# Kernel tuning notes

Hardware: AMD Instinct MI355X
Metric: run time of the kernel (lower is better)

## Reference

```python
import jax, jax.numpy as jnp
import numpy as np

E, T, D_IN, D_H = 8, 2048, 2048, 5632


def setup_inputs() -> dict:
    key = jax.random.key(0)
    kx, kg, kd, ku = jax.random.split(key, 4)
    scale = 0.02  # init_std-like scaling for weights
    return {
        "x": jax.random.normal(kx, (E, T, D_IN), dtype=jnp.float32),
        "gate_proj": jax.random.normal(kg, (E, D_IN, D_H), dtype=jnp.float32) * scale,
        "down_proj": jax.random.normal(kd, (E, D_IN, D_H), dtype=jnp.float32) * scale,
        "up_proj": jax.random.normal(ku, (E, D_H, D_IN), dtype=jnp.float32) * scale,
        "tokens_per_expert": T,
    }


def reference(x, gate_proj, down_proj, up_proj, tokens_per_expert):
    # ep_size=1: dispatch/combine are identity. Grouped SwiGLU per expert.
    # x: [E, T, d_in]; gate/down: [E, d_in, d_h]; up: [E, d_h, d_in]
    g = jnp.einsum('etd,edh->eth', x, gate_proj)
    u = jnp.einsum('etd,edh->eth', x, down_proj)
    h = jax.nn.silu(g) * u  # [E, T, d_h]
    out = jnp.einsum('eth,ehd->etd', h, up_proj)  # [E, T, d_in]
    return out
```

## Files before the change

### kernel.cpp

```cpp
#include <hip/hip_runtime.h>
#include <hip/hip_bf16.h>


#define NEXP 8
#define TT   2048
#define DIN  2048
#define DH   5632

using short8 = __attribute__((ext_vector_type(8))) short;
using f32x4  = __attribute__((ext_vector_type(4))) float;

static __device__ __forceinline__ float bf2f(unsigned short u) {
    return __uint_as_float(((unsigned int)u) << 16);
}
static __device__ __forceinline__ unsigned short f2bf(float f) {
    unsigned int i = __float_as_uint(f);
    return (unsigned short)((i + 0x7FFFu + ((i >> 16) & 1u)) >> 16);
}
static __device__ __forceinline__ void gld16(const void* g, void* l) {
    __builtin_amdgcn_global_load_lds(
        (const __attribute__((address_space(1))) void*)g,
        (__attribute__((address_space(3))) void*)l, 16, 0, 0);
}

__global__ __launch_bounds__(512, 2) void gemm_gu(
    const unsigned short* __restrict__ Xb,
    const unsigned short* __restrict__ Wgt,
    const unsigned short* __restrict__ Wdt,
    unsigned short* __restrict__ Hb)
{
    __shared__ __align__(16) unsigned short lds[65536];

    const int tid  = threadIdx.x;
    const int wave = tid >> 6, lane = tid & 63;
    const int l15 = lane & 15, l4 = lane >> 4;
    const int wr = wave >> 2, wc = wave & 3;

    const int bid = blockIdx.x;
    const int e   = bid & 7;
    const int cu  = bid >> 3;
    const int m0  = (cu & 7) * 256;
    const int nb  = cu >> 3;

    const int K = DIN;

    const unsigned short* Ae = Xb  + (size_t)e * TT * DIN;
    const unsigned short* Gbase = Wgt + (size_t)e * DH * DIN;
    const unsigned short* Dbase = Wdt + (size_t)e * DH * DIN;
    unsigned short* He = Hb + (size_t)e * TT * DH;

    const int c0 = tid, c1 = 512 + tid;
    const int cs0 = c0 ^ ((c0 >> 3) & 7), cs1 = c1 ^ ((c1 >> 3) & 7);
    const int row0 = cs0 >> 3, col0 = (cs0 & 7) * 8;
    const int row1 = cs1 >> 3, col1 = (cs1 & 7) * 8;

    int ibA[4][2], ibB[2][2];
#pragma unroll
    for (int s = 0; s < 4; ++s)
#pragma unroll
        for (int ks = 0; ks < 2; ++ks) {
            const int r = wr * 64 + s * 16 + l15;
            ibA[s][ks] = (r * 128 + ks * 64 + l4 * 16) ^ ((r & 7) << 4);
        }
#pragma unroll
    for (int s = 0; s < 2; ++s)
#pragma unroll
        for (int ks = 0; ks < 2; ++ks) {
            const int r = wc * 32 + s * 16 + l15;
            ibB[s][ks] = (r * 128 + ks * 64 + l4 * 16) ^ ((r & 7) << 4);
        }

    f32x4 acc[8][4] = {};
    short8 Aq[4][2], Gq[2][2], Dq[2][2];

    auto stageA = [&](int ro, int kk, int slot) {
        gld16(Ae + (size_t)(m0 + ro + row0) * K + (kk + col0), &lds[slot * 8192 + wave * 512]);
        gld16(Ae + (size_t)(m0 + ro + row1) * K + (kk + col1), &lds[slot * 8192 + 4096 + wave * 512]);
    };
    auto stageW = [&](const unsigned short* p, int kk, int slot) {
        gld16(p + (size_t)row0 * K + (kk + col0), &lds[slot * 8192 + wave * 512]);
        gld16(p + (size_t)row1 * K + (kk + col1), &lds[slot * 8192 + 4096 + wave * 512]);
    };

    const size_t NSTEP = (size_t)512 * K;
    const unsigned short* Gc = Gbase + (size_t)(nb * 128) * K;
    const unsigned short* Dc = Dbase + (size_t)(nb * 128) * K;

    stageA(0, 0, 0);  stageW(Gc, 0, 1);  stageW(Dc, 0, 2);  stageA(128, 0, 3);
    stageA(0, 64, 4); stageW(Gc, 64, 5); stageW(Dc, 64, 6);
    asm volatile("s_waitcnt vmcnt(6)" ::: "memory");
    asm volatile("s_barrier" ::: "memory");

    const char* ldsc = (const char*)lds;
    for (int i = 0; i < 11; ++i) {
        const unsigned short* Gn = Gc + NSTEP;
        const unsigned short* Dn = Dc + NSTEP;
        for (int t = 0; t < 32; ++t) {
            const int g = (i << 5) + t;
            const int sA0 = ((4 * g + 0) & 7) * 16384;
            const int sG  = ((4 * g + 1) & 7) * 16384;
            const int sD  = ((4 * g + 2) & 7) * 16384;
            const int sA1 = ((4 * g + 3) & 7) * 16384;

#pragma unroll
            for (int s = 0; s < 4; ++s) {
                Aq[s][0] = *(const short8*)(ldsc + sA0 + ibA[s][0]);
                Aq[s][1] = *(const short8*)(ldsc + sA0 + ibA[s][1]);
            }
#pragma unroll
            for (int s = 0; s < 2; ++s) {
                Gq[s][0] = *(const short8*)(ldsc + sG + ibB[s][0]);
                Gq[s][1] = *(const short8*)(ldsc + sG + ibB[s][1]);
            }
            if (i < 10 || t + 1 < 32)
                stageA(128, ((t + 1) & 31) * 64, (4 * g + 7) & 7);
            asm volatile("s_barrier" ::: "memory");
            asm volatile("s_waitcnt lgkmcnt(0)" ::: "memory");
            __builtin_amdgcn_sched_barrier(0);
            __builtin_amdgcn_s_setprio(1);
#pragma unroll
            for (int m = 0; m < 4; ++m)
#pragma unroll
                for (int n = 0; n < 2; ++n) {
                    acc[m][n] = __builtin_amdgcn_mfma_f32_16x16x32_bf16(Aq[m][0], Gq[n][0], acc[m][n], 0, 0, 0);
                    acc[m][n] = __builtin_amdgcn_mfma_f32_16x16x32_bf16(Aq[m][1], Gq[n][1], acc[m][n], 0, 0, 0);
                }
            __builtin_amdgcn_s_setprio(0);
            asm volatile("s_barrier" ::: "memory");

#pragma unroll
            for (int s = 0; s < 2; ++s) {
                Dq[s][0] = *(const short8*)(ldsc + sD + ibB[s][0]);
                Dq[s][1] = *(const short8*)(ldsc + sD + ibB[s][1]);
            }
            if (i < 10 || t + 2 < 32)
                stageA(0, ((t + 2) & 31) * 64, (4 * g + 8) & 7);
            asm volatile("s_barrier" ::: "memory");
            asm volatile("s_waitcnt lgkmcnt(0)" ::: "memory");
            __builtin_amdgcn_sched_barrier(0);
            __builtin_amdgcn_s_setprio(1);
#pragma unroll
            for (int m = 0; m < 4; ++m)
#pragma unroll
                for (int n = 0; n < 2; ++n) {
                    acc[m][2 + n] = __builtin_amdgcn_mfma_f32_16x16x32_bf16(Aq[m][0], Dq[n][0], acc[m][2 + n], 0, 0, 0);
                    acc[m][2 + n] = __builtin_amdgcn_mfma_f32_16x16x32_bf16(Aq[m][1], Dq[n][1], acc[m][2 + n], 0, 0, 0);
                }
            __builtin_amdgcn_s_setprio(0);
            asm volatile("s_barrier" ::: "memory");

#pragma unroll
            for (int s = 0; s < 4; ++s) {
                Aq[s][0] = *(const short8*)(ldsc + sA1 + ibA[s][0]);
                Aq[s][1] = *(const short8*)(ldsc + sA1 + ibA[s][1]);
            }
            if (i < 10 || t + 2 < 32)
                stageW((t + 2 < 32) ? Gc : Gn, ((t + 2) & 31) * 64, (4 * g + 9) & 7);
            asm volatile("s_barrier" ::: "memory");
            asm volatile("s_waitcnt lgkmcnt(0)" ::: "memory");
            __builtin_amdgcn_sched_barrier(0);
            __builtin_amdgcn_s_setprio(1);
#pragma unroll
            for (int m = 0; m < 4; ++m)
#pragma unroll
                for (int n = 0; n < 2; ++n) {
                    acc[4 + m][2 + n] = __builtin_amdgcn_mfma_f32_16x16x32_bf16(Aq[m][0], Dq[n][0], acc[4 + m][2 + n], 0, 0, 0);
                    acc[4 + m][2 + n] = __builtin_amdgcn_mfma_f32_16x16x32_bf16(Aq[m][1], Dq[n][1], acc[4 + m][2 + n], 0, 0, 0);
                }
            __builtin_amdgcn_s_setprio(0);
            asm volatile("s_barrier" ::: "memory");

            if (i < 10 || t + 2 < 32)
                stageW((t + 2 < 32) ? Dc : Dn, ((t + 2) & 31) * 64, (4 * g + 10) & 7);
            asm volatile("s_barrier" ::: "memory");
            __builtin_amdgcn_s_setprio(1);
#pragma unroll
            for (int m = 0; m < 4; ++m)
#pragma unroll
                for (int n = 0; n < 2; ++n) {
                    acc[4 + m][n] = __builtin_amdgcn_mfma_f32_16x16x32_bf16(Aq[m][0], Gq[n][0], acc[4 + m][n], 0, 0, 0);
                    acc[4 + m][n] = __builtin_amdgcn_mfma_f32_16x16x32_bf16(Aq[m][1], Gq[n][1], acc[4 + m][n], 0, 0, 0);
                }
            __builtin_amdgcn_s_setprio(0);
            if (g < 350)       asm volatile("s_waitcnt vmcnt(6)" ::: "memory");
            else if (g == 350) asm volatile("s_waitcnt vmcnt(0)" ::: "memory");
            asm volatile("s_barrier" ::: "memory");
        }

        const int n0i = (4 * i + nb) * 128;
#pragma unroll
        for (int fm = 0; fm < 8; ++fm) {
            const int row_b = m0 + (fm >> 2) * 128 + wr * 64 + (fm & 3) * 16 + l4 * 4;
#pragma unroll
            for (int nr = 0; nr < 2; ++nr) {
                const int col = n0i + wc * 32 + nr * 16 + l15;
#pragma unroll
                for (int j = 0; j < 4; ++j) {
                    const float gv = acc[fm][nr][j];
                    const float uv = acc[fm][2 + nr][j];
                    const float h = gv / (1.f + __expf(-gv)) * uv;
                    He[(size_t)(row_b + j) * DH + col] = f2bf(h);
                }
            }
        }
#pragma unroll
        for (int m = 0; m < 8; ++m)
#pragma unroll
            for (int n = 0; n < 4; ++n)
                acc[m][n] = (f32x4){0.f, 0.f, 0.f, 0.f};
        Gc = Gn; Dc = Dn;
    }
}

__global__ __launch_bounds__(512, 2) void gemm_out(
    const unsigned short* __restrict__ Ab,
    const unsigned short* __restrict__ Btb,
    float* __restrict__ Cf)
{
    __shared__ __align__(16) unsigned short lds[65536];

    const int tid  = threadIdx.x;
    const int wave = tid >> 6, lane = tid & 63;
    const int l15 = lane & 15, l4 = lane >> 4;
    const int wr = wave >> 2, wc = wave & 3;

    const int bid = blockIdx.x;
    const int e   = bid & 7;
    const int cu  = bid >> 3;
    const int m0  = (cu & 7) * 256;
    const int nb  = cu >> 3;

    const int N = DIN, K = DH, NT = K >> 6;
    const unsigned short* Ae = Ab  + (size_t)e * TT * DH;
    const unsigned short* Bbase = Btb + (size_t)e * DIN * DH;

    const int c0 = tid, c1 = 512 + tid;
    const int cs0 = c0 ^ ((c0 >> 3) & 7), cs1 = c1 ^ ((c1 >> 3) & 7);
    const int row0 = cs0 >> 3, col0 = (cs0 & 7) * 8;
    const int row1 = cs1 >> 3, col1 = (cs1 & 7) * 8;

    int ibA[4][2], ibB[2][2];
#pragma unroll
    for (int s = 0; s < 4; ++s)
#pragma unroll
        for (int ks = 0; ks < 2; ++ks) {
            const int r = wr * 64 + s * 16 + l15;
            ibA[s][ks] = (r * 128 + ks * 64 + l4 * 16) ^ ((r & 7) << 4);
        }
#pragma unroll
    for (int s = 0; s < 2; ++s)
#pragma unroll
        for (int ks = 0; ks < 2; ++ks) {
            const int r = wc * 32 + s * 16 + l15;
            ibB[s][ks] = (r * 128 + ks * 64 + l4 * 16) ^ ((r & 7) << 4);
        }

    f32x4 acc[8][4] = {};
    short8 Aq[4][2], B0q[2][2], B1q[2][2];

    auto stageA = [&](int ro, int kk, int slot) {
        gld16(Ae + (size_t)(m0 + ro + row0) * K + (kk + col0), &lds[slot * 8192 + wave * 512]);
        gld16(Ae + (size_t)(m0 + ro + row1) * K + (kk + col1), &lds[slot * 8192 + 4096 + wave * 512]);
    };
    auto stageB = [&](const unsigned short* base, int co, int kk, int slot) {
        gld16(base + (size_t)(co + row0) * K + (kk + col0), &lds[slot * 8192 + wave * 512]);
        gld16(base + (size_t)(co + row1) * K + (kk + col1), &lds[slot * 8192 + 4096 + wave * 512]);
    };

    const size_t NSTEP = (size_t)1024 * K;
    const unsigned short* Bc = Bbase + (size_t)(nb * 256) * K;

    stageA(0, 0, 0); stageB(Bc, 0, 0, 1); stageB(Bc, 128, 0, 2); stageA(128, 0, 3);
    stageA(0, 64, 4); stageB(Bc, 0, 64, 5); stageB(Bc, 128, 64, 6);
    asm volatile("s_waitcnt vmcnt(6)" ::: "memory");
    asm volatile("s_barrier" ::: "memory");

    const char* ldsc = (const char*)lds;
    for (int i = 0; i < 2; ++i) {
        const unsigned short* Bn = Bc + NSTEP;
        for (int t = 0; t < 88; ++t) {
            const int g = i * 88 + t;
            const int sA0 = ((4 * g + 0) & 7) * 16384;
            const int sB0 = ((4 * g + 1) & 7) * 16384;
            const int sB1 = ((4 * g + 2) & 7) * 16384;
            const int sA1 = ((4 * g + 3) & 7) * 16384;

#pragma unroll
            for (int s = 0; s < 4; ++s) {
                Aq[s][0] = *(const short8*)(ldsc + sA0 + ibA[s][0]);
                Aq[s][1] = *(const short8*)(ldsc + sA0 + ibA[s][1]);
            }
#pragma unroll
            for (int s = 0; s < 2; ++s) {
                B0q[s][0] = *(const short8*)(ldsc + sB0 + ibB[s][0]);
                B0q[s][1] = *(const short8*)(ldsc + sB0 + ibB[s][1]);
            }
            {
                const int tt = t + 1;
                if (i < 1 || tt < 88)
                    stageA(128, (tt >= 88 ? tt - 88 : tt) * 64, (4 * g + 7) & 7);
            }
            asm volatile("s_barrier" ::: "memory");
            asm volatile("s_waitcnt lgkmcnt(0)" ::: "memory");
            __builtin_amdgcn_sched_barrier(0);
            __builtin_amdgcn_s_setprio(1);
#pragma unroll
            for (int m = 0; m < 4; ++m)
#pragma unroll
                for (int n = 0; n < 2; ++n) {
                    acc[m][n] = __builtin_amdgcn_mfma_f32_16x16x32_bf16(Aq[m][0], B0q[n][0], acc[m][n], 0, 0, 0);
                    acc[m][n] = __builtin_amdgcn_mfma_f32_16x16x32_bf16(Aq[m][1], B0q[n][1], acc[m][n], 0, 0, 0);
                }
            __builtin_amdgcn_s_setprio(0);
            asm volatile("s_barrier" ::: "memory");

#pragma unroll
            for (int s = 0; s < 2; ++s) {
                B1q[s][0] = *(const short8*)(ldsc + sB1 + ibB[s][0]);
                B1q[s][1] = *(const short8*)(ldsc + sB1 + ibB[s][1]);
            }
            {
                const int tt = t + 2;
                if (i < 1 || tt < 88)
                    stageA(0, (tt >= 88 ? tt - 88 : tt) * 64, (4 * g + 8) & 7);
            }
            asm volatile("s_barrier" ::: "memory");
            asm volatile("s_waitcnt lgkmcnt(0)" ::: "memory");
            __builtin_amdgcn_sched_barrier(0);
            __builtin_amdgcn_s_setprio(1);
#pragma unroll
            for (int m = 0; m < 4; ++m)
#pragma unroll
                for (int n = 0; n < 2; ++n) {
                    acc[m][2 + n] = __builtin_amdgcn_mfma_f32_16x16x32_bf16(Aq[m][0], B1q[n][0], acc[m][2 + n], 0, 0, 0);
                    acc[m][2 + n] = __builtin_amdgcn_mfma_f32_16x16x32_bf16(Aq[m][1], B1q[n][1], acc[m][2 + n], 0, 0, 0);
                }
            __builtin_amdgcn_s_setprio(0);
            asm volatile("s_barrier" ::: "memory");

#pragma unroll
            for (int s = 0; s < 4; ++s) {
                Aq[s][0] = *(const short8*)(ldsc + sA1 + ibA[s][0]);
                Aq[s][1] = *(const short8*)(ldsc + sA1 + ibA[s][1]);
            }
            {
                const int tt = t + 2;
                if (i < 1 || tt < 88)
                    stageB((tt >= 88 ? Bn : Bc), 0, (tt >= 88 ? tt - 88 : tt) * 64, (4 * g + 9) & 7);
            }
            asm volatile("s_barrier" ::: "memory");
            asm volatile("s_waitcnt lgkmcnt(0)" ::: "memory");
            __builtin_amdgcn_sched_barrier(0);
            __builtin_amdgcn_s_setprio(1);
#pragma unroll
            for (int m = 0; m < 4; ++m)
#pragma unroll
                for (int n = 0; n < 2; ++n) {
                    acc[4 + m][2 + n] = __builtin_amdgcn_mfma_f32_16x16x32_bf16(Aq[m][0], B1q[n][0], acc[4 + m][2 + n], 0, 0, 0);
                    acc[4 + m][2 + n] = __builtin_amdgcn_mfma_f32_16x16x32_bf16(Aq[m][1], B1q[n][1], acc[4 + m][2 + n], 0, 0, 0);
                }
            __builtin_amdgcn_s_setprio(0);
            asm volatile("s_barrier" ::: "memory");

            {
                const int tt = t + 2;
                if (i < 1 || tt < 88)
                    stageB((tt >= 88 ? Bn : Bc), 128, (tt >= 88 ? tt - 88 : tt) * 64, (4 * g + 10) & 7);
            }
            asm volatile("s_barrier" ::: "memory");
            __builtin_amdgcn_s_setprio(1);
#pragma unroll
            for (int m = 0; m < 4; ++m)
#pragma unroll
                for (int n = 0; n < 2; ++n) {
                    acc[4 + m][n] = __builtin_amdgcn_mfma_f32_16x16x32_bf16(Aq[m][0], B0q[n][0], acc[4 + m][n], 0, 0, 0);
                    acc[4 + m][n] = __builtin_amdgcn_mfma_f32_16x16x32_bf16(Aq[m][1], B0q[n][1], acc[4 + m][n], 0, 0, 0);
                }
            __builtin_amdgcn_s_setprio(0);
            if (g < 174)       asm volatile("s_waitcnt vmcnt(6)" ::: "memory");
            else if (g == 174) asm volatile("s_waitcnt vmcnt(0)" ::: "memory");
            asm volatile("s_barrier" ::: "memory");
        }

        const int n0i = (4 * i + nb) * 256;
        float* Ce = Cf + (size_t)e * TT * DIN;
#pragma unroll
        for (int fm = 0; fm < 8; ++fm) {
            const int row_b = (fm >> 2) * 128 + wr * 64 + (fm & 3) * 16 + l4 * 4;
#pragma unroll
            for (int fn = 0; fn < 4; ++fn) {
                const int col = n0i + (fn >> 1) * 128 + wc * 32 + (fn & 1) * 16 + l15;
#pragma unroll
                for (int j = 0; j < 4; ++j)
                    Ce[(size_t)(m0 + row_b + j) * N + col] = acc[fm][fn][j];
            }
        }
#pragma unroll
        for (int m = 0; m < 8; ++m)
#pragma unroll
            for (int n = 0; n < 4; ++n)
                acc[m][n] = (f32x4){0.f, 0.f, 0.f, 0.f};
        Bc = Bn;
    }
}

__global__ __launch_bounds__(256) void transpose_f32_bf16(
    const float* __restrict__ in, unsigned short* __restrict__ out,
    int R, int C, size_t ies, size_t oes)
{
    in  += (size_t)blockIdx.z * ies;
    out += (size_t)blockIdx.z * oes;
    __shared__ unsigned short t[64][65];
    const int tid = threadIdx.x;
    const int lr = tid >> 4, lc = (tid & 15) * 4;
    const int r0 = blockIdx.y * 64, c0 = blockIdx.x * 64;
#pragma unroll
    for (int i = 0; i < 4; ++i) {
        const int row = lr + i * 16;
        const float4 v = *(const float4*)(in + (size_t)(r0 + row) * C + c0 + lc);
        t[row][lc + 0] = f2bf(v.x); t[row][lc + 1] = f2bf(v.y);
        t[row][lc + 2] = f2bf(v.z); t[row][lc + 3] = f2bf(v.w);
    }
    __syncthreads();
#pragma unroll
    for (int i = 0; i < 4; ++i) {
        const int crow = lr + i * 16;
        ushort4 wv;
        wv.x = t[lc + 0][crow]; wv.y = t[lc + 1][crow];
        wv.z = t[lc + 2][crow]; wv.w = t[lc + 3][crow];
        *(ushort4*)(out + (size_t)(c0 + crow) * R + r0 + lc) = wv;
    }
}

__global__ __launch_bounds__(256) void conv_f32_bf16(
    const float* __restrict__ in, unsigned short* __restrict__ out, int n4)
{
    int i = blockIdx.x * 256 + threadIdx.x;
    const int stride = gridDim.x * 256;
    for (; i < n4; i += stride) {
        const float4 v = ((const float4*)in)[i];
        ushort4 wv;
        wv.x = f2bf(v.x); wv.y = f2bf(v.y); wv.z = f2bf(v.z); wv.w = f2bf(v.w);
        ((ushort4*)out)[i] = wv;
    }
}

extern "C" void kernel_launch(void* const* d_in, const int* in_sizes, int n_in,
                              void* d_out, int out_size, void* d_ws, size_t ws_size,
                              hipStream_t stream)
{
    const float* x  = (const float*)d_in[0];
    const float* wg = (const float*)d_in[1];
    const float* wd = (const float*)d_in[2];
    const float* wu = (const float*)d_in[3];
    float* out = (float*)d_out;

    const size_t XSZ = (size_t)TT * DIN;
    const size_t WSZ = (size_t)DIN * DH;
    unsigned short* xb  = (unsigned short*)d_ws;
    unsigned short* wgt = xb  + (size_t)NEXP * XSZ;
    unsigned short* wdt = wgt + (size_t)NEXP * WSZ;
    unsigned short* hb  = wdt + (size_t)NEXP * WSZ;

    conv_f32_bf16<<<4096, 256, 0, stream>>>(x, xb, (int)(NEXP * XSZ / 4));
    transpose_f32_bf16<<<dim3(DH / 64, DIN / 64, NEXP), 256, 0, stream>>>(
        wg, wgt, DIN, DH, WSZ, WSZ);
    transpose_f32_bf16<<<dim3(DH / 64, DIN / 64, NEXP), 256, 0, stream>>>(
        wd, wdt, DIN, DH, WSZ, WSZ);
    gemm_gu<<<256, 512, 0, stream>>>(xb, wgt, wdt, hb);
    transpose_f32_bf16<<<dim3(DIN / 64, DH / 64, NEXP), 256, 0, stream>>>(
        wu, wgt, DH, DIN, WSZ, WSZ);
    gemm_out<<<256, 512, 0, stream>>>(hb, wgt, out);
}
```

Baseline: 1.297 ms.

## Grow LDS ring to ten slots and cut per-step barriers from eight to two

Both GEMM kernels move from an 8-slot to a 10-slot LDS ring buffer, indexed by a running modulo-10 counter. The extra slots let the next global-to-LDS stages be issued without waiting for readers. Both B fragments are now loaded together at the start of each step, and the MFMA phases are merged, so only two workgroup barriers remain per step instead of eight. This raises LDS per block from 128 KB to 160 KB, which may stop two 512-thread blocks fitting per CU. It also depends on the widened ring for correctness against write-after-read hazards.

```diff
diff --git a/kernel.cpp b/kernel.cpp
--- a/kernel.cpp
+++ b/kernel.cpp
@@ -10,9 +10,6 @@
 using short8 = __attribute__((ext_vector_type(8))) short;
 using f32x4  = __attribute__((ext_vector_type(4))) float;
 
-static __device__ __forceinline__ float bf2f(unsigned short u) {
-    return __uint_as_float(((unsigned int)u) << 16);
-}
 static __device__ __forceinline__ unsigned short f2bf(float f) {
     unsigned int i = __float_as_uint(f);
     return (unsigned short)((i + 0x7FFFu + ((i >> 16) & 1u)) >> 16);
@@ -29,7 +26,7 @@
     const unsigned short* __restrict__ Wdt,
     unsigned short* __restrict__ Hb)
 {
-    __shared__ __align__(16) unsigned short lds[65536];
+    __shared__ __align__(16) unsigned short lds[81920];
 
     const int tid  = threadIdx.x;
     const int wave = tid >> 6, lane = tid & 63;
@@ -45,8 +42,6 @@
     const int K = DIN;
 
     const unsigned short* Ae = Xb  + (size_t)e * TT * DIN;
-    const unsigned short* Gbase = Wgt + (size_t)e * DH * DIN;
-    const unsigned short* Dbase = Wdt + (size_t)e * DH * DIN;
     unsigned short* He = Hb + (size_t)e * TT * DH;
 
     const int c0 = tid, c1 = 512 + tid;
@@ -73,34 +68,41 @@
     f32x4 acc[8][4] = {};
     short8 Aq[4][2], Gq[2][2], Dq[2][2];
 
-    auto stageA = [&](int ro, int kk, int slot) {
-        gld16(Ae + (size_t)(m0 + ro + row0) * K + (kk + col0), &lds[slot * 8192 + wave * 512]);
-        gld16(Ae + (size_t)(m0 + ro + row1) * K + (kk + col1), &lds[slot * 8192 + 4096 + wave * 512]);
+    char* ldsb = (char*)lds;
+    auto stageA = [&](int ro, int kk, int so) {
+        gld16(Ae + (size_t)(m0 + ro + row0) * K + (kk + col0), ldsb + so + wave * 1024);
+        gld16(Ae + (size_t)(m0 + ro + row1) * K + (kk + col1), ldsb + so + 8192 + wave * 1024);
     };
-    auto stageW = [&](const unsigned short* p, int kk, int slot) {
-        gld16(p + (size_t)row0 * K + (kk + col0), &lds[slot * 8192 + wave * 512]);
-        gld16(p + (size_t)row1 * K + (kk + col1), &lds[slot * 8192 + 4096 + wave * 512]);
+    auto stageW = [&](const unsigned short* p, int kk, int so) {
+        gld16(p + (size_t)row0 * K + (kk + col0), ldsb + so + wave * 1024);
+        gld16(p + (size_t)row1 * K + (kk + col1), ldsb + so + 8192 + wave * 1024);
     };
+    auto w10 = [](int x) { return x >= 10 ? x - 10 : x; };
 
     const size_t NSTEP = (size_t)512 * K;
-    const unsigned short* Gc = Gbase + (size_t)(nb * 128) * K;
-    const unsigned short* Dc = Dbase + (size_t)(nb * 128) * K;
-
-    stageA(0, 0, 0);  stageW(Gc, 0, 1);  stageW(Dc, 0, 2);  stageA(128, 0, 3);
-    stageA(0, 64, 4); stageW(Gc, 64, 5); stageW(Dc, 64, 6);
+    const unsigned short* Gc = Wgt + (size_t)e * DH * DIN + (size_t)(nb * 128) * K;
+    const unsigned short* Dc = Wdt + (size_t)e * DH * DIN + (size_t)(nb * 128) * K;
+
+    stageA(0, 0, 0 << 14);  stageW(Gc, 0, 1 << 14);  stageW(Dc, 0, 2 << 14);  stageA(128, 0, 3 << 14);
+    stageA(0, 64, 4 << 14); stageW(Gc, 64, 5 << 14); stageW(Dc, 64, 6 << 14);
     asm volatile("s_waitcnt vmcnt(6)" ::: "memory");
     asm volatile("s_barrier" ::: "memory");
 
     const char* ldsc = (const char*)lds;
+    int q = 0;
     for (int i = 0; i < 11; ++i) {
         const unsigned short* Gn = Gc + NSTEP;
         const unsigned short* Dn = Dc + NSTEP;
         for (int t = 0; t < 32; ++t) {
             const int g = (i << 5) + t;
-            const int sA0 = ((4 * g + 0) & 7) * 16384;
-            const int sG  = ((4 * g + 1) & 7) * 16384;
-            const int sD  = ((4 * g + 2) & 7) * 16384;
-            const int sA1 = ((4 * g + 3) & 7) * 16384;
+            const int sA0 = q << 14;
+            const int sG  = w10(q + 1) << 14;
+            const int sD  = w10(q + 2) << 14;
+            const int sA1 = w10(q + 3) << 14;
+            const int stA1 = w10(q + 7) << 14;
+            const int stA0 = w10(q + 8) << 14;
+            const int stG  = w10(q + 9) << 14;
+            const int stD  = sA0;
 
 #pragma unroll
             for (int s = 0; s < 4; ++s) {
@@ -111,10 +113,11 @@
             for (int s = 0; s < 2; ++s) {
                 Gq[s][0] = *(const short8*)(ldsc + sG + ibB[s][0]);
                 Gq[s][1] = *(const short8*)(ldsc + sG + ibB[s][1]);
+                Dq[s][0] = *(const short8*)(ldsc + sD + ibB[s][0]);
+                Dq[s][1] = *(const short8*)(ldsc + sD + ibB[s][1]);
             }
             if (i < 10 || t + 1 < 32)
-                stageA(128, ((t + 1) & 31) * 64, (4 * g + 7) & 7);
-            asm volatile("s_barrier" ::: "memory");
+                stageA(128, ((t + 1) & 31) * 64, stA1);
             asm volatile("s_waitcnt lgkmcnt(0)" ::: "memory");
             __builtin_amdgcn_sched_barrier(0);
             __builtin_amdgcn_s_setprio(1);
@@ -126,18 +129,8 @@
                     acc[m][n] = __builtin_amdgcn_mfma_f32_16x16x32_bf16(Aq[m][1], Gq[n][1], acc[m][n], 0, 0, 0);
                 }
             __builtin_amdgcn_s_setprio(0);
-            asm volatile("s_barrier" ::: "memory");
-
-#pragma unroll
-            for (int s = 0; s < 2; ++s) {
-                Dq[s][0] = *(const short8*)(ldsc + sD + ibB[s][0]);
-                Dq[s][1] = *(const short8*)(ldsc + sD + ibB[s][1]);
-            }
             if (i < 10 || t + 2 < 32)
-                stageA(0, ((t + 2) & 31) * 64, (4 * g + 8) & 7);
-            asm volatile("s_barrier" ::: "memory");
-            asm volatile("s_waitcnt lgkmcnt(0)" ::: "memory");
-            __builtin_amdgcn_sched_barrier(0);
+                stageA(0, ((t + 2) & 31) * 64, stA0);
             __builtin_amdgcn_s_setprio(1);
 #pragma unroll
             for (int m = 0; m < 4; ++m)
@@ -147,16 +140,13 @@
                     acc[m][2 + n] = __builtin_amdgcn_mfma_f32_16x16x32_bf16(Aq[m][1], Dq[n][1], acc[m][2 + n], 0, 0, 0);
                 }
             __builtin_amdgcn_s_setprio(0);
-            asm volatile("s_barrier" ::: "memory");
-
 #pragma unroll
             for (int s = 0; s < 4; ++s) {
                 Aq[s][0] = *(const short8*)(ldsc + sA1 + ibA[s][0]);
                 Aq[s][1] = *(const short8*)(ldsc + sA1 + ibA[s][1]);
             }
             if (i < 10 || t + 2 < 32)
-                stageW((t + 2 < 32) ? Gc : Gn, ((t + 2) & 31) * 64, (4 * g + 9) & 7);
-            asm volatile("s_barrier" ::: "memory");
+                stageW((t + 2 < 32) ? Gc : Gn, ((t + 2) & 31) * 64, stG);
             asm volatile("s_waitcnt lgkmcnt(0)" ::: "memory");
             __builtin_amdgcn_sched_barrier(0);
             __builtin_amdgcn_s_setprio(1);
@@ -167,13 +157,6 @@
                     acc[4 + m][2 + n] = __builtin_amdgcn_mfma_f32_16x16x32_bf16(Aq[m][0], Dq[n][0], acc[4 + m][2 + n], 0, 0, 0);
                     acc[4 + m][2 + n] = __builtin_amdgcn_mfma_f32_16x16x32_bf16(Aq[m][1], Dq[n][1], acc[4 + m][2 + n], 0, 0, 0);
                 }
-            __builtin_amdgcn_s_setprio(0);
-            asm volatile("s_barrier" ::: "memory");
-
-            if (i < 10 || t + 2 < 32)
-                stageW((t + 2 < 32) ? Dc : Dn, ((t + 2) & 31) * 64, (4 * g + 10) & 7);
-            asm volatile("s_barrier" ::: "memory");
-            __builtin_amdgcn_s_setprio(1);
 #pragma unroll
             for (int m = 0; m < 4; ++m)
 #pragma unroll
@@ -182,9 +165,13 @@
                     acc[4 + m][n] = __builtin_amdgcn_mfma_f32_16x16x32_bf16(Aq[m][1], Gq[n][1], acc[4 + m][n], 0, 0, 0);
                 }
             __builtin_amdgcn_s_setprio(0);
+            asm volatile("s_barrier" ::: "memory");
+            if (i < 10 || t + 2 < 32)
+                stageW((t + 2 < 32) ? Dc : Dn, ((t + 2) & 31) * 64, stD);
             if (g < 350)       asm volatile("s_waitcnt vmcnt(6)" ::: "memory");
             else if (g == 350) asm volatile("s_waitcnt vmcnt(0)" ::: "memory");
             asm volatile("s_barrier" ::: "memory");
+            q = w10(q + 4);
         }
 
         const int n0i = (4 * i + nb) * 128;
@@ -217,7 +204,7 @@
     const unsigned short* __restrict__ Btb,
     float* __restrict__ Cf)
 {
-    __shared__ __align__(16) unsigned short lds[65536];
+    __shared__ __align__(16) unsigned short lds[81920];
 
     const int tid  = threadIdx.x;
     const int wave = tid >> 6, lane = tid & 63;
@@ -230,9 +217,8 @@
     const int m0  = (cu & 7) * 256;
     const int nb  = cu >> 3;
 
-    const int N = DIN, K = DH, NT = K >> 6;
+    const int N = DIN, K = DH;
     const unsigned short* Ae = Ab  + (size_t)e * TT * DH;
-    const unsigned short* Bbase = Btb + (size_t)e * DIN * DH;
 
     const int c0 = tid, c1 = 512 + tid;
     const int cs0 = c0 ^ ((c0 >> 3) & 7), cs1 = c1 ^ ((c1 >> 3) & 7);
@@ -258,32 +244,39 @@
     f32x4 acc[8][4] = {};
     short8 Aq[4][2], B0q[2][2], B1q[2][2];
 
-    auto stageA = [&](int ro, int kk, int slot) {
-        gld16(Ae + (size_t)(m0 + ro + row0) * K + (kk + col0), &lds[slot * 8192 + wave * 512]);
-        gld16(Ae + (size_t)(m0 + ro + row1) * K + (kk + col1), &lds[slot * 8192 + 4096 + wave * 512]);
+    char* ldsb = (char*)lds;
+    auto stageA = [&](int ro, int kk, int so) {
+        gld16(Ae + (size_t)(m0 + ro + row0) * K + (kk + col0), ldsb + so + wave * 1024);
+        gld16(Ae + (size_t)(m0 + ro + row1) * K + (kk + col1), ldsb + so + 8192 + wave * 1024);
     };
-    auto stageB = [&](const unsigned short* base, int co, int kk, int slot) {
-        gld16(base + (size_t)(co + row0) * K + (kk + col0), &lds[slot * 8192 + wave * 512]);
-        gld16(base + (size_t)(co + row1) * K + (kk + col1), &lds[slot * 8192 + 4096 + wave * 512]);
+    auto stageB = [&](const unsigned short* base, int co, int kk, int so) {
+        gld16(base + (size_t)(co + row0) * K + (kk + col0), ldsb + so + wave * 1024);
+        gld16(base + (size_t)(co + row1) * K + (kk + col1), ldsb + so + 8192 + wave * 1024);
     };
+    auto w10 = [](int x) { return x >= 10 ? x - 10 : x; };
 
     const size_t NSTEP = (size_t)1024 * K;
-    const unsigned short* Bc = Bbase + (size_t)(nb * 256) * K;
-
-    stageA(0, 0, 0); stageB(Bc, 0, 0, 1); stageB(Bc, 128, 0, 2); stageA(128, 0, 3);
-    stageA(0, 64, 4); stageB(Bc, 0, 64, 5); stageB(Bc, 128, 64, 6);
+    const unsigned short* Bc = Btb + (size_t)e * DIN * DH + (size_t)(nb * 256) * K;
+
+    stageA(0, 0, 0 << 14); stageB(Bc, 0, 0, 1 << 14); stageB(Bc, 128, 0, 2 << 14); stageA(128, 0, 3 << 14);
+    stageA(0, 64, 4 << 14); stageB(Bc, 0, 64, 5 << 14); stageB(Bc, 128, 64, 6 << 14);
     asm volatile("s_waitcnt vmcnt(6)" ::: "memory");
     asm volatile("s_barrier" ::: "memory");
 
     const char* ldsc = (const char*)lds;
+    int q = 0;
     for (int i = 0; i < 2; ++i) {
         const unsigned short* Bn = Bc + NSTEP;
         for (int t = 0; t < 88; ++t) {
             const int g = i * 88 + t;
-            const int sA0 = ((4 * g + 0) & 7) * 16384;
-            const int sB0 = ((4 * g + 1) & 7) * 16384;
-            const int sB1 = ((4 * g + 2) & 7) * 16384;
-            const int sA1 = ((4 * g + 3) & 7) * 16384;
+            const int sA0 = q << 14;
+            const int sB0 = w10(q + 1) << 14;
+            const int sB1 = w10(q + 2) << 14;
+            const int sA1 = w10(q + 3) << 14;
+            const int stA1 = w10(q + 7) << 14;
+            const int stA0 = w10(q + 8) << 14;
+            const int stB0 = w10(q + 9) << 14;
+            const int stB1 = sA0;
 
 #pragma unroll
             for (int s = 0; s < 4; ++s) {
@@ -294,13 +287,14 @@
             for (int s = 0; s < 2; ++s) {
                 B0q[s][0] = *(const short8*)(ldsc + sB0 + ibB[s][0]);
                 B0q[s][1] = *(const short8*)(ldsc + sB0 + ibB[s][1]);
+                B1q[s][0] = *(const short8*)(ldsc + sB1 + ibB[s][0]);
+                B1q[s][1] = *(const short8*)(ldsc + sB1 + ibB[s][1]);
             }
             {
                 const int tt = t + 1;
                 if (i < 1 || tt < 88)
-                    stageA(128, (tt >= 88 ? tt - 88 : tt) * 64, (4 * g + 7) & 7);
-            }
-            asm volatile("s_barrier" ::: "memory");
+                    stageA(128, (tt >= 88 ? tt - 88 : tt) * 64, stA1);
+            }
             asm volatile("s_waitcnt lgkmcnt(0)" ::: "memory");
             __builtin_amdgcn_sched_barrier(0);
             __builtin_amdgcn_s_setprio(1);
@@ -312,21 +306,11 @@
                     acc[m][n] = __builtin_amdgcn_mfma_f32_16x16x32_bf16(Aq[m][1], B0q[n][1], acc[m][n], 0, 0, 0);
                 }
             __builtin_amdgcn_s_setprio(0);
-            asm volatile("s_barrier" ::: "memory");
-
-#pragma unroll
-            for (int s = 0; s < 2; ++s) {
-                B1q[s][0] = *(const short8*)(ldsc + sB1 + ibB[s][0]);
-                B1q[s][1] = *(const short8*)(ldsc + sB1 + ibB[s][1]);
-            }
             {
                 const int tt = t + 2;
                 if (i < 1 || tt < 88)
-                    stageA(0, (tt >= 88 ? tt - 88 : tt) * 64, (4 * g + 8) & 7);
-            }
-            asm volatile("s_barrier" ::: "memory");
-            asm volatile("s_waitcnt lgkmcnt(0)" ::: "memory");
-            __builtin_amdgcn_sched_barrier(0);
+                    stageA(0, (tt >= 88 ? tt - 88 : tt) * 64, stA0);
+            }
             __builtin_amdgcn_s_setprio(1);
 #pragma unroll
             for (int m = 0; m < 4; ++m)
@@ -336,8 +320,6 @@
                     acc[m][2 + n] = __builtin_amdgcn_mfma_f32_16x16x32_bf16(Aq[m][1], B1q[n][1], acc[m][2 + n], 0, 0, 0);
                 }
             __builtin_amdgcn_s_setprio(0);
-            asm volatile("s_barrier" ::: "memory");
-
 #pragma unroll
             for (int s = 0; s < 4; ++s) {
                 Aq[s][0] = *(const short8*)(ldsc + sA1 + ibA[s][0]);
@@ -346,9 +328,8 @@
             {
                 const int tt = t + 2;
                 if (i < 1 || tt < 88)
-                    stageB((tt >= 88 ? Bn : Bc), 0, (tt >= 88 ? tt - 88 : tt) * 64, (4 * g + 9) & 7);
-            }
-            asm volatile("s_barrier" ::: "memory");
+                    stageB((tt >= 88 ? Bn : Bc), 0, (tt >= 88 ? tt - 88 : tt) * 64, stB0);
+            }
             asm volatile("s_waitcnt lgkmcnt(0)" ::: "memory");
             __builtin_amdgcn_sched_barrier(0);
             __builtin_amdgcn_s_setprio(1);
@@ -359,27 +340,24 @@
                     acc[4 + m][2 + n] = __builtin_amdgcn_mfma_f32_16x16x32_bf16(Aq[m][0], B1q[n][0], acc[4 + m][2 + n], 0, 0, 0);
                     acc[4 + m][2 + n] = __builtin_amdgcn_mfma_f32_16x16x32_bf16(Aq[m][1], B1q[n][1], acc[4 + m][2 + n], 0, 0, 0);
                 }
+#pragma unroll
+            for (int m = 0; m < 4; ++m)
+#pragma unroll
+                for (int n = 0; n < 2; ++n) {
+                    acc[4 + m][n] = __builtin_amdgcn_mfma_f32_16x16x32_bf16(Aq[m][0], B0q[n][0], acc[4 + m][n], 0, 0, 0);
+                    acc[4 + m][n] = __builtin_amdgcn_mfma_f32_16x16x32_bf16(Aq[m][1], B0q[n][1], acc[4 + m][n], 0, 0, 0);
+                }
             __builtin_amdgcn_s_setprio(0);
             asm volatile("s_barrier" ::: "memory");
-
             {
                 const int tt = t + 2;
                 if (i < 1 || tt < 88)
-                    stageB((tt >= 88 ? Bn : Bc), 128, (tt >= 88 ? tt - 88 : tt) * 64, (4 * g + 10) & 7);
-            }
-            asm volatile("s_barrier" ::: "memory");
-            __builtin_amdgcn_s_setprio(1);
-#pragma unroll
-            for (int m = 0; m < 4; ++m)
-#pragma unroll
-                for (int n = 0; n < 2; ++n) {
-                    acc[4 + m][n] = __builtin_amdgcn_mfma_f32_16x16x32_bf16(Aq[m][0], B0q[n][0], acc[4 + m][n], 0, 0, 0);
-                    acc[4 + m][n] = __builtin_amdgcn_mfma_f32_16x16x32_bf16(Aq[m][1], B0q[n][1], acc[4 + m][n], 0, 0, 0);
-                }
-            __builtin_amdgcn_s_setprio(0);
+                    stageB((tt >= 88 ? Bn : Bc), 128, (tt >= 88 ? tt - 88 : tt) * 64, stB1);
+            }
             if (g < 174)       asm volatile("s_waitcnt vmcnt(6)" ::: "memory");
             else if (g == 174) asm volatile("s_waitcnt vmcnt(0)" ::: "memory");
             asm volatile("s_barrier" ::: "memory");
+            q = w10(q + 4);
         }
 
         const int n0i = (4 * i + nb) * 256;
```

After: 1.292 ms. Within noise of the previous version (-0.4%).
